# Optimization experiments

Hardware: AMD Instinct MI355X
Metric: run time of the kernel (lower is better)

## Reference

```python
import jax, jax.numpy as jnp
import numpy as np
import math

B, S, H, NH = 8, 2048, 256, 4
DH = H // NH
EPS = 1e-12


def setup_inputs() -> dict:
    key = jax.random.key(0)
    ks = jax.random.split(key, 20)
    g = lambda k, shape: (jax.random.normal(k, shape, jnp.float32) * 0.02)
    inp = {
        "hidden": jax.random.normal(ks[0], (B, S, H), jnp.float32),
        "Wq": g(ks[1], (H, H)), "bq": jnp.zeros((H,), jnp.float32),
        "Wk": g(ks[2], (H, H)), "bk": jnp.zeros((H,), jnp.float32),
        "Wv": g(ks[3], (H, H)), "bv": jnp.zeros((H,), jnp.float32),
        "Wo": g(ks[4], (H, H)), "bo": jnp.zeros((H,), jnp.float32),
        "W1": g(ks[5], (4 * H, H)), "b1": jnp.zeros((4 * H,), jnp.float32),
        "W2": g(ks[6], (H, 4 * H)), "b2": jnp.zeros((H,), jnp.float32),
        "ln1_w": jnp.ones((H,), jnp.float32), "ln1_b": jnp.zeros((H,), jnp.float32),
        "ln2_w": jnp.ones((H,), jnp.float32), "ln2_b": jnp.zeros((H,), jnp.float32),
        "mask": jax.random.randint(ks[7], (B, S), 0, 2, jnp.int32),
    }
    return inp


def _layernorm(x, w, b):
    u = x.mean(-1, keepdims=True)
    s = ((x - u) ** 2).mean(-1, keepdims=True)
    return w * (x - u) / jnp.sqrt(s + EPS) + b


def _gelu_tanh(h):
    return 0.5 * h * (1.0 + jnp.tanh(math.sqrt(2.0 / math.pi) * (h + 0.044715 * h ** 3)))


def _block(hidden, mask, Wq, bq, Wk, bk, Wv, bv, Wo, bo, W1, b1, W2, b2,
           ln1_w, ln1_b, ln2_w, ln2_b):
    # --- attention sublayer (pre-norm + residual) ---
    x = _layernorm(hidden, ln1_w, ln1_b)
    def heads(W, b):  # [B,S,H] -> [B,NH,S,DH]
        return (x @ W.T + b).reshape(B, S, NH, DH).transpose(0, 2, 1, 3)
    q, k, v = heads(Wq, bq), heads(Wk, bk), heads(Wv, bv)
    corr = jnp.einsum("bhqd,bhkd->bhqk", q, k) / math.sqrt(DH)
    # torch code masks QUERY rows: mask [B,S] broadcast over heads and keys
    corr = jnp.where(mask[:, None, :, None] == 0, -1e9, corr)
    prob = jax.nn.softmax(corr, axis=-1)
    attn = jnp.einsum("bhqk,bhkd->bhqd", prob, v)
    attn = attn.transpose(0, 2, 1, 3).reshape(B, S, H) @ Wo.T + bo
    hidden = hidden + attn
    # --- FFN sublayer (pre-norm + residual) ---
    y = _layernorm(hidden, ln2_w, ln2_b)
    h1 = y @ W1.T + b1
    ff = _gelu_tanh(h1) @ W2.T + b2
    return hidden + ff


def reference(hidden, Wq, bq, Wk, bk, Wv, bv, Wo, bo, W1, b1, W2, b2,
              ln1_w, ln1_b, ln2_w, ln2_b, mask):
    return _block(hidden, mask, Wq, bq, Wk, bk, Wv, bv, Wo, bo,
                  W1, b1, W2, b2, ln1_w, ln1_b, ln2_w, ln2_b)
```

## Files before the change

kernel.cpp:

```cpp
#include <hip/hip_runtime.h>
#include <hip/hip_bf16.h>
#include <cstdint>
#include <cstddef>

constexpr int CB  = 8;
constexpr int CS  = 2048;
constexpr int CH  = 256;
constexpr int CNH = 4;
constexpr int CDH = 64;
constexpr int CT  = CB * CS;

typedef __attribute__((ext_vector_type(8))) __bf16 bf16x8;
typedef __attribute__((ext_vector_type(4))) float  f32x4;

__device__ __forceinline__ float b2f(unsigned short u) {
    union { float f; unsigned int i; } v; v.i = ((unsigned int)u) << 16; return v.f;
}
__device__ __forceinline__ unsigned short f2b(float f) {
    union { float f; unsigned int i; } v; v.f = f;
    unsigned int r = v.i + 0x7FFFu + ((v.i >> 16) & 1u);
    return (unsigned short)(r >> 16);
}
__device__ __forceinline__ unsigned short f2b_fast(float f) {
    union { float f; unsigned int i; } v; v.f = f;
    return (unsigned short)((v.i + 0x8000u) >> 16);
}
__device__ __forceinline__ float fexp2(float x) {
#if __has_builtin(__builtin_amdgcn_exp2f)
    return __builtin_amdgcn_exp2f(x);
#else
    float r; asm("v_exp_f32 %0, %1" : "=v"(r) : "v"(x)); return r;
#endif
}
__device__ __forceinline__ f32x4 mfma16(bf16x8 a, bf16x8 b, f32x4 c) {
    return __builtin_amdgcn_mfma_f32_16x16x32_bf16(a, b, c, 0, 0, 0);
}

#define GLOAD_LDS16(gptr, lptr)                                                        \
    __builtin_amdgcn_global_load_lds((const __attribute__((address_space(1))) void*)(gptr), \
                                     (__attribute__((address_space(3))) void*)(lptr), 16, 0, 0)

#define QSCALE 0.1803368801111204f

__global__ __launch_bounds__(256) void detect_kernel(
    const unsigned short* __restrict__ h, int* __restrict__ flag)
{
    __shared__ int s_bad;
    const int tid = threadIdx.x;
    if (tid == 0) s_bad = 0;
    __syncthreads();
    bool bad = false;
    for (int i = tid; i < 2048; i += 256) {
        float v = b2f(h[i]);
        if (!(fabsf(v) < 1e25f)) bad = true;
    }
    if (bad) s_bad = 1;
    __syncthreads();
    if (tid == 0) *flag = s_bad;
}

struct CvtArgs6  { const void* src[6];  void* dst[6];  int n[6]; };
struct CvtArgs11 { const void* src[11]; void* dst[11]; int n[11]; };

__global__ __launch_bounds__(256) void cvt_to_bf16_k(const int* __restrict__ flag, CvtArgs6 a)
{
    const int seg = blockIdx.y, n = a.n[seg];
    const bool inf32 = (*flag != 0);
    const float* sf = (const float*)a.src[seg];
    const unsigned short* sb = (const unsigned short*)a.src[seg];
    unsigned short* d = (unsigned short*)a.dst[seg];
    for (int i = (blockIdx.x * 256 + threadIdx.x) * 4; i < n; i += gridDim.x * 1024) {
        ushort4 o;
        if (inf32) {
            float4 v = *(const float4*)(sf + i);
            o.x = f2b(v.x); o.y = f2b(v.y); o.z = f2b(v.z); o.w = f2b(v.w);
        } else {
            o = *(const ushort4*)(sb + i);
        }
        *(ushort4*)(d + i) = o;
    }
}

__global__ __launch_bounds__(256) void cvt_to_f32_k(const int* __restrict__ flag, CvtArgs11 a)
{
    const int seg = blockIdx.y, n = a.n[seg];
    const bool inf32 = (*flag != 0);
    const float* sf = (const float*)a.src[seg];
    const unsigned short* sb = (const unsigned short*)a.src[seg];
    float* d = (float*)a.dst[seg];
    for (int i = (blockIdx.x * 256 + threadIdx.x) * 4; i < n; i += gridDim.x * 1024) {
        float4 o;
        if (inf32) {
            o = *(const float4*)(sf + i);
        } else {
            ushort4 v = *(const ushort4*)(sb + i);
            o.x = b2f(v.x); o.y = b2f(v.y); o.z = b2f(v.z); o.w = b2f(v.w);
        }
        *(float4*)(d + i) = o;
    }
}

__global__ __launch_bounds__(256) void ln_kernel(
    const float* __restrict__ x, const float* __restrict__ w,
    const float* __restrict__ b, unsigned short* __restrict__ out)
{
    const int wave = threadIdx.x >> 6, lane = threadIdx.x & 63;
    const int token = blockIdx.x * 4 + wave;
    const int c = lane * 4;
    const size_t rowo = (size_t)token * CH + c;
    float4 u = *(const float4*)(x + rowo);
    float v0 = u.x, v1 = u.y, v2 = u.z, v3 = u.w;
    float s = v0 + v1 + v2 + v3;
    float q = v0*v0 + v1*v1 + v2*v2 + v3*v3;
    #pragma unroll
    for (int m = 1; m < 64; m <<= 1) { s += __shfl_xor(s, m, 64); q += __shfl_xor(q, m, 64); }
    float mean = s * (1.0f/256.0f);
    float var  = q * (1.0f/256.0f) - mean*mean;
    float inv  = rsqrtf(var + 1e-12f);
    float4 ww = *(const float4*)(w + c);
    float4 bb = *(const float4*)(b + c);
    ushort4 o;
    o.x = f2b(ww.x * (v0-mean)*inv + bb.x);
    o.y = f2b(ww.y * (v1-mean)*inv + bb.y);
    o.z = f2b(ww.z * (v2-mean)*inv + bb.z);
    o.w = f2b(ww.w * (v3-mean)*inv + bb.w);
    *(ushort4*)(out + rowo) = o;
}

template<bool GELU, bool RESID, bool HEADSTORE, bool OUTF32, bool OUTDYN>
__device__ __forceinline__ void gemm_core(
    const unsigned short* __restrict__ A, const unsigned short* __restrict__ W,
    const float* __restrict__ bias, const float* __restrict__ resid,
    void* __restrict__ out, const int* __restrict__ flag,
    int K, int N, int m0, int n0, float oscale)
{
    __shared__ __align__(16) unsigned short lA[128*32];
    __shared__ __align__(16) unsigned short lB[128*32];
    const int tid  = threadIdx.x;
    const int lane = tid & 63;
    const int wave = tid >> 6;
    const int wr = (wave >> 1) * 64;
    const int wc = (wave & 1) * 64;
    const int g = lane >> 4, r16 = lane & 15;
    const int lrow = lane >> 2;
    const int lch  = lane & 3;

    const f32x4 zero = {0.f, 0.f, 0.f, 0.f};
    f32x4 acc[4][4];
    #pragma unroll
    for (int m = 0; m < 4; ++m)
        #pragma unroll
        for (int n = 0; n < 4; ++n) acc[m][n] = zero;

    for (int k0 = 0; k0 < K; k0 += 32) {
        #pragma unroll
        for (int i = 0; i < 2; ++i) {
            int chunk = wave + i * 4;
            int row = chunk * 16 + lrow;
            const unsigned short* ga = A + (size_t)(m0 + row) * K + k0 + lch * 8;
            GLOAD_LDS16(ga, &lA[chunk * 512]);
            const unsigned short* gw = W + (size_t)(n0 + row) * K + k0 + lch * 8;
            GLOAD_LDS16(gw, &lB[chunk * 512]);
        }
        __syncthreads();
        bf16x8 af[4], wf[4];
        #pragma unroll
        for (int m = 0; m < 4; ++m) af[m] = *(const bf16x8*)&lA[(wr + m*16 + r16) * 32 + g * 8];
        #pragma unroll
        for (int n = 0; n < 4; ++n) wf[n] = *(const bf16x8*)&lB[(wc + n*16 + r16) * 32 + g * 8];
        #pragma unroll
        for (int m = 0; m < 4; ++m)
            #pragma unroll
            for (int n = 0; n < 4; ++n)
                acc[m][n] = mfma16(af[m], wf[n], acc[m][n]);
        __syncthreads();
    }

    const bool of32dyn = OUTDYN ? (*flag != 0) : false;
    #pragma unroll
    for (int n = 0; n < 4; ++n) {
        int col = n0 + wc + n*16 + r16;
        float bv = bias[col];
        #pragma unroll
        for (int m = 0; m < 4; ++m) {
            int row0 = m0 + wr + m*16 + g*4;
            #pragma unroll
            for (int r = 0; r < 4; ++r) {
                int row = row0 + r;
                float v = (acc[m][n][r] + bv) * oscale;
                if (GELU) {
                    float a = 0.79788456080286541f * (v + 0.044715f * v * v * v);
                    v = v * (1.0f / (1.0f + __expf(-2.0f * a)));
                }
                if (RESID) v += resid[(size_t)row * N + col];
                size_t oidx;
                if (HEADSTORE) {
                    int hh = col >> 6, d = col & 63;
                    int bb = row >> 11, ss = row & 2047;
                    oidx = ((((size_t)bb * CNH + hh) * CS) + ss) * CDH + d;
                } else {
                    oidx = (size_t)row * N + col;
                }
                if (OUTF32)      ((float*)out)[oidx] = v;
                else if (OUTDYN) {
                    if (of32dyn) ((float*)out)[oidx] = v;
                    else         ((unsigned short*)out)[oidx] = f2b(v);
                }
                else             ((unsigned short*)out)[oidx] = f2b(v);
            }
        }
    }
}

__global__ __launch_bounds__(256) void k_qkv(
    const unsigned short* __restrict__ xhat,
    const unsigned short* Wq, const float* bq, unsigned short* q,
    const unsigned short* Wk, const float* bk, unsigned short* k,
    const unsigned short* Wv, const float* bv, unsigned short* v)
{
    const unsigned short* W  = blockIdx.z == 0 ? Wq : (blockIdx.z == 1 ? Wk : Wv);
    const float*          bi = blockIdx.z == 0 ? bq : (blockIdx.z == 1 ? bk : bv);
    unsigned short*       o  = blockIdx.z == 0 ? q  : (blockIdx.z == 1 ? k  : v);
    const float osc = blockIdx.z == 0 ? QSCALE : 1.0f;
    gemm_core<false, false, true, false, false>(xhat, W, bi, nullptr, o, nullptr,
                                                CH, CH, blockIdx.x * 128, blockIdx.y * 128, osc);
}

__global__ __launch_bounds__(256) void k_oproj(
    const unsigned short* __restrict__ A, const unsigned short* __restrict__ W,
    const float* __restrict__ bias, const float* __restrict__ resid,
    float* __restrict__ out)
{
    gemm_core<false, true, false, true, false>(A, W, bias, resid, out, nullptr,
                                               CH, CH, blockIdx.x * 128, blockIdx.y * 128, 1.0f);
}

__global__ __launch_bounds__(256) void k_ffn1(
    const unsigned short* __restrict__ A, const unsigned short* __restrict__ W,
    const float* __restrict__ bias, unsigned short* __restrict__ out)
{
    gemm_core<true, false, false, false, false>(A, W, bias, nullptr, out, nullptr,
                                                CH, 4*CH, blockIdx.x * 128, blockIdx.y * 128, 1.0f);
}

__global__ __launch_bounds__(256) void k_ffn2(
    const unsigned short* __restrict__ A, const unsigned short* __restrict__ W,
    const float* __restrict__ bias, const float* __restrict__ resid,
    void* __restrict__ out, const int* __restrict__ flag)
{
    gemm_core<false, true, false, false, true>(A, W, bias, resid, out, flag,
                                               4*CH, CH, blockIdx.x * 128, blockIdx.y * 128, 1.0f);
}

__global__ __launch_bounds__(256) void vtrans_kernel(
    const unsigned short* __restrict__ v, unsigned short* __restrict__ vt)
{
    __shared__ unsigned short T[64 * 72];
    const int bh = blockIdx.y, s0 = blockIdx.x * 64, tid = threadIdx.x;
    const size_t ibase = (size_t)bh * CS * CDH;
    const size_t obase = (size_t)bh * CDH * CS;
    #pragma unroll
    for (int i = 0; i < 2; ++i) {
        int t2 = tid + i * 256;
        int row = t2 >> 3, ch = t2 & 7;
        uint4 dv = *(const uint4*)(v + ibase + (size_t)(s0 + row) * CDH + ch * 8);
        *(uint4*)&T[row * 72 + ch * 8] = dv;
    }
    __syncthreads();
    #pragma unroll
    for (int i = 0; i < 2; ++i) {
        int t2 = tid + i * 256;
        int d = t2 >> 3, ch = t2 & 7;
        unsigned short tmp[8];
        #pragma unroll
        for (int j = 0; j < 8; ++j) tmp[j] = T[(ch * 8 + j) * 72 + d];
        *(uint4*)(vt + obase + (size_t)d * CS + s0 + ch * 8) = *(uint4*)tmp;
    }
}

__global__ __launch_bounds__(512, 4) void attn_kernel(
    const unsigned short* __restrict__ Q, const unsigned short* __restrict__ Kp,
    const unsigned short* __restrict__ Vt, const int* __restrict__ mask,
    unsigned short* __restrict__ out)
{
    __shared__ __align__(16) unsigned short Qs[128 * 64];
    __shared__ __align__(16) unsigned short Ks[128 * 64];
    __shared__ __align__(16) unsigned short Vs[64 * 128];
    __shared__ __align__(16) unsigned short Ps[128 * 128];

    const int tid = threadIdx.x, lane = tid & 63, wave = tid >> 6;
    const int bh = blockIdx.y, bb = bh >> 2, hh = bh & 3;
    const int q0 = blockIdx.x * 128;
    const size_t baseQ = (size_t)bh * CS * CDH;
    const size_t baseT = (size_t)bh * CDH * CS;

    const int g = lane >> 4, r16 = lane & 15;
    const int wq = wave * 16;
    const int swz = (r16 & 7) << 4;

    #pragma unroll
    for (int i = 0; i < 2; ++i) {
        int t2 = tid + i * 512;
        int row = t2 >> 3, ch = t2 & 7;
        uint4 dv = *(const uint4*)(Q + baseQ + (size_t)(q0 + row) * CDH + ch * 8);
        if (mask[bb * CS + q0 + row] == 0) { dv.x = 0; dv.y = 0; dv.z = 0; dv.w = 0; }
        *(uint4*)((char*)Qs + row * 128 + ((ch * 16) ^ ((row & 7) << 4))) = dv;
    }

    f32x4 o_acc[4];
    float psum[4];
    #pragma unroll
    for (int n = 0; n < 4; ++n) o_acc[n] = (f32x4){0.f, 0.f, 0.f, 0.f};
    #pragma unroll
    for (int r = 0; r < 4; ++r) psum[r] = 0.f;

    const int kr0 = tid >> 3,  kc0 = tid & 7;
    const int kr1 = kr0 + 64;
    const int vd0 = tid >> 4,  vc0 = tid & 15;
    const int vd1 = vd0 + 32;
    char* kdstA = (char*)Ks + kr0 * 128 + ((kc0 * 16) ^ ((kr0 & 7) << 4));
    char* kdstB = (char*)Ks + kr1 * 128 + ((kc0 * 16) ^ ((kr1 & 7) << 4));
    char* vdstA = (char*)Vs + vd0 * 256 + ((vc0 * 16) ^ ((vd0 & 7) << 4));
    char* vdstB = (char*)Vs + vd1 * 256 + ((vc0 * 16) ^ ((vd1 & 7) << 4));

    uint4 kva, kvb, vva, vvb;
    kva = *(const uint4*)(Kp + baseQ + (size_t)kr0 * CDH + kc0 * 8);
    kvb = *(const uint4*)(Kp + baseQ + (size_t)kr1 * CDH + kc0 * 8);
    vva = *(const uint4*)(Vt + baseT + (size_t)vd0 * CS + vc0 * 8);
    vvb = *(const uint4*)(Vt + baseT + (size_t)vd1 * CS + vc0 * 8);

    for (int kt = 0; kt < CS; kt += 128) {
        *(uint4*)kdstA = kva;  *(uint4*)kdstB = kvb;
        *(uint4*)vdstA = vva;  *(uint4*)vdstB = vvb;
        __syncthreads();
        if (kt + 128 < CS) {
            kva = *(const uint4*)(Kp + baseQ + (size_t)(kt + 128 + kr0) * CDH + kc0 * 8);
            kvb = *(const uint4*)(Kp + baseQ + (size_t)(kt + 128 + kr1) * CDH + kc0 * 8);
            vva = *(const uint4*)(Vt + baseT + (size_t)vd0 * CS + (kt + 128) + vc0 * 8);
            vvb = *(const uint4*)(Vt + baseT + (size_t)vd1 * CS + (kt + 128) + vc0 * 8);
        }

        f32x4 s_acc[8];
        #pragma unroll
        for (int n = 0; n < 8; ++n) s_acc[n] = (f32x4){0.f, 0.f, 0.f, 0.f};
        __builtin_amdgcn_s_setprio(1);
        #pragma unroll
        for (int kk = 0; kk < 2; ++kk) {
            bf16x8 aq = *(const bf16x8*)((char*)Qs + (wq + r16) * 128 + ((kk*64 + g*16) ^ swz));
            #pragma unroll
            for (int n = 0; n < 8; ++n) {
                bf16x8 bk2 = *(const bf16x8*)((char*)Ks + (n*16 + r16) * 128 + ((kk*64 + g*16) ^ swz));
                s_acc[n] = mfma16(aq, bk2, s_acc[n]);
            }
        }
        __builtin_amdgcn_s_setprio(0);

        #pragma unroll
        for (int r = 0; r < 4; ++r) {
            const int rloc = wq + g * 4 + r;
            char* prow = (char*)Ps + rloc * 256;
            const int pswz = (rloc & 7) << 4;
            float acc = 0.f;
            #pragma unroll
            for (int n = 0; n < 8; ++n) {
                float p = fexp2(s_acc[n][r]);
                acc += p;
                *(unsigned short*)(prow + (((n*16 + r16) * 2) ^ pswz)) = f2b_fast(p);
            }
            psum[r] += acc;
        }

        __builtin_amdgcn_s_setprio(1);
        #pragma unroll
        for (int kk = 0; kk < 4; ++kk) {
            bf16x8 ap = *(const bf16x8*)((char*)Ps + (wq + r16) * 256 + ((kk*64 + g*16) ^ swz));
            #pragma unroll
            for (int n = 0; n < 4; ++n) {
                bf16x8 bv2 = *(const bf16x8*)((char*)Vs + (n*16 + r16) * 256 + ((kk*64 + g*16) ^ swz));
                o_acc[n] = mfma16(ap, bv2, o_acc[n]);
            }
        }
        __builtin_amdgcn_s_setprio(0);
        __syncthreads();
    }

    #pragma unroll
    for (int r = 0; r < 4; ++r) {
        float l = psum[r];
        #pragma unroll
        for (int d = 1; d < 16; d <<= 1) l += __shfl_xor(l, d, 64);
        float inv = 1.0f / l;
        const int rloc = wq + g * 4 + r;
        #pragma unroll
        for (int n = 0; n < 4; ++n)
            out[((size_t)(bb * CS + q0 + rloc)) * CH + hh * CDH + n*16 + r16] =
                f2b(o_acc[n][r] * inv);
    }
}

extern "C" void kernel_launch(void* const* d_in, const int* in_sizes, int n_in,
                              void* d_out, int out_size, void* d_ws, size_t ws_size,
                              hipStream_t stream)
{
    const void* hidden = d_in[0];
    const void* Wq = d_in[1];  const void* bq = d_in[2];
    const void* Wk = d_in[3];  const void* bk = d_in[4];
    const void* Wv = d_in[5];  const void* bv = d_in[6];
    const void* Wo = d_in[7];  const void* bo = d_in[8];
    const void* W1 = d_in[9];  const void* b1 = d_in[10];
    const void* W2 = d_in[11]; const void* b2 = d_in[12];
    const void* ln1w = d_in[13]; const void* ln1b = d_in[14];
    const void* ln2w = d_in[15]; const void* ln2b = d_in[16];
    const int* mask = (const int*)d_in[17];

    char* ws = (char*)d_ws;
    const size_t KB = 1u << 10, MB = 1u << 20;
    int*            flag  = (int*)ws;
    float*          bqf   = (float*)(ws + 4*KB);
    float*          bkf   = (float*)(ws + 8*KB);
    float*          bvf   = (float*)(ws + 12*KB);
    float*          bof   = (float*)(ws + 16*KB);
    float*          b1f   = (float*)(ws + 20*KB);
    float*          b2f_  = (float*)(ws + 28*KB);
    float*          ln1wf = (float*)(ws + 32*KB);
    float*          ln1bf = (float*)(ws + 36*KB);
    float*          ln2wf = (float*)(ws + 40*KB);
    float*          ln2bf = (float*)(ws + 44*KB);
    unsigned short* Wqb   = (unsigned short*)(ws + 1*MB);
    unsigned short* Wkb   = (unsigned short*)(ws + 1*MB + 256*KB);
    unsigned short* Wvb   = (unsigned short*)(ws + 1*MB + 512*KB);
    unsigned short* Wob   = (unsigned short*)(ws + 1*MB + 768*KB);
    unsigned short* W1b   = (unsigned short*)(ws + 2*MB);
    unsigned short* W2b   = (unsigned short*)(ws + 2*MB + 512*KB);
    float*          hf32  = (float*)(ws + 3*MB);
    unsigned short* xhat  = (unsigned short*)(ws + 19*MB);
    unsigned short* qb    = (unsigned short*)(ws + 27*MB);
    unsigned short* kb    = (unsigned short*)(ws + 35*MB);
    unsigned short* vb    = (unsigned short*)(ws + 43*MB);
    unsigned short* attnb = xhat;
    float*          hid2f = (float*)(ws + 35*MB);
    unsigned short* vtb   = (unsigned short*)(ws + 51*MB);
    unsigned short* yhat  = qb;
    unsigned short* h1g   = (unsigned short*)(ws + 51*MB);

    dim3 blk(256);
    detect_kernel<<<1, blk, 0, stream>>>((const unsigned short*)hidden, flag);

    CvtArgs6 cw;
    cw.src[0]=Wq;  cw.dst[0]=Wqb; cw.n[0]=CH*CH;
    cw.src[1]=Wk;  cw.dst[1]=Wkb; cw.n[1]=CH*CH;
    cw.src[2]=Wv;  cw.dst[2]=Wvb; cw.n[2]=CH*CH;
    cw.src[3]=Wo;  cw.dst[3]=Wob; cw.n[3]=CH*CH;
    cw.src[4]=W1;  cw.dst[4]=W1b; cw.n[4]=4*CH*CH;
    cw.src[5]=W2;  cw.dst[5]=W2b; cw.n[5]=4*CH*CH;
    cvt_to_bf16_k<<<dim3(64, 6), blk, 0, stream>>>(flag, cw);

    CvtArgs11 cf;
    cf.src[0]=hidden; cf.dst[0]=hf32;  cf.n[0]=CT*CH;
    cf.src[1]=bq;     cf.dst[1]=bqf;   cf.n[1]=CH;
    cf.src[2]=bk;     cf.dst[2]=bkf;   cf.n[2]=CH;
    cf.src[3]=bv;     cf.dst[3]=bvf;   cf.n[3]=CH;
    cf.src[4]=bo;     cf.dst[4]=bof;   cf.n[4]=CH;
    cf.src[5]=b1;     cf.dst[5]=b1f;   cf.n[5]=4*CH;
    cf.src[6]=b2;     cf.dst[6]=b2f_;  cf.n[6]=CH;
    cf.src[7]=ln1w;   cf.dst[7]=ln1wf; cf.n[7]=CH;
    cf.src[8]=ln1b;   cf.dst[8]=ln1bf; cf.n[8]=CH;
    cf.src[9]=ln2w;   cf.dst[9]=ln2wf; cf.n[9]=CH;
    cf.src[10]=ln2b;  cf.dst[10]=ln2bf;cf.n[10]=CH;
    cvt_to_f32_k<<<dim3(512, 11), blk, 0, stream>>>(flag, cf);

    ln_kernel<<<CT / 4, blk, 0, stream>>>(hf32, ln1wf, ln1bf, xhat);
    k_qkv<<<dim3(CT / 128, CH / 128, 3), blk, 0, stream>>>(xhat, Wqb, bqf, qb,
                                                           Wkb, bkf, kb, Wvb, bvf, vb);
    vtrans_kernel<<<dim3(CS / 64, CB * CNH), blk, 0, stream>>>(vb, vtb);
    attn_kernel<<<dim3(CS / 128, CB * CNH), dim3(512), 0, stream>>>(qb, kb, vtb, mask, attnb);
    k_oproj<<<dim3(CT / 128, CH / 128), blk, 0, stream>>>(attnb, Wob, bof, hf32, hid2f);
    ln_kernel<<<CT / 4, blk, 0, stream>>>(hid2f, ln2wf, ln2bf, yhat);
    k_ffn1<<<dim3(CT / 128, (4 * CH) / 128), blk, 0, stream>>>(yhat, W1b, b1f, h1g);
    k_ffn2<<<dim3(CT / 128, CH / 128), blk, 0, stream>>>(h1g, W2b, b2f_, hid2f,
                                                         d_out, flag);
}
```

Before: 173.2 us.

## Rewrite attention kernel with 32x32 MFMA, register P, and async LDS double buffering

Restructures the attention kernel to use 32x32x16 MFMAs, computing S^T so each wave keeps Q in registers. Waves are split into pairs sharing query rows, each pair covering half the key tile. P is repacked in registers with permlane32_swap instead of going through an LDS round trip. K and V tiles are double-buffered via global_load_lds direct-to-LDS copies. Partial O and row sums from the two key halves are combined through LDS at the end, which adds an epilogue reduction and changes the LDS layout to an unswizzled packed form that may cause bank conflicts.

```diff
diff --git a/kernel.cpp b/kernel.cpp
--- a/kernel.cpp
+++ b/kernel.cpp
@@ -10,8 +10,10 @@
 constexpr int CDH = 64;
 constexpr int CT  = CB * CS;
 
-typedef __attribute__((ext_vector_type(8))) __bf16 bf16x8;
-typedef __attribute__((ext_vector_type(4))) float  f32x4;
+typedef __attribute__((ext_vector_type(8)))  __bf16 bf16x8;
+typedef __attribute__((ext_vector_type(4)))  float  f32x4;
+typedef __attribute__((ext_vector_type(16))) float  f32x16;
+typedef __attribute__((ext_vector_type(2)))  int    i32x2;
 
 __device__ __forceinline__ float b2f(unsigned short u) {
     union { float f; unsigned int i; } v; v.i = ((unsigned int)u) << 16; return v.f;
@@ -24,6 +26,9 @@
 __device__ __forceinline__ unsigned short f2b_fast(float f) {
     union { float f; unsigned int i; } v; v.f = f;
     return (unsigned short)((v.i + 0x8000u) >> 16);
+}
+__device__ __forceinline__ unsigned int packbf(float a, float b) {
+    return (unsigned int)f2b_fast(a) | ((unsigned int)f2b_fast(b) << 16);
 }
 __device__ __forceinline__ float fexp2(float x) {
 #if __has_builtin(__builtin_amdgcn_exp2f)
@@ -34,6 +39,15 @@
 }
 __device__ __forceinline__ f32x4 mfma16(bf16x8 a, bf16x8 b, f32x4 c) {
     return __builtin_amdgcn_mfma_f32_16x16x32_bf16(a, b, c, 0, 0, 0);
+}
+__device__ __forceinline__ f32x16 mfma32(bf16x8 a, bf16x8 b, f32x16 c) {
+    return __builtin_amdgcn_mfma_f32_32x32x16_bf16(a, b, c, 0, 0, 0);
+}
+__device__ __forceinline__ f32x16 zero16() {
+    f32x16 z;
+    #pragma unroll
+    for (int i = 0; i < 16; ++i) z[i] = 0.f;
+    return z;
 }
 
 #define GLOAD_LDS16(gptr, lptr)                                                        \
@@ -283,119 +297,127 @@
     const unsigned short* __restrict__ Vt, const int* __restrict__ mask,
     unsigned short* __restrict__ out)
 {
-    __shared__ __align__(16) unsigned short Qs[128 * 64];
-    __shared__ __align__(16) unsigned short Ks[128 * 64];
-    __shared__ __align__(16) unsigned short Vs[64 * 128];
-    __shared__ __align__(16) unsigned short Ps[128 * 128];
+    __shared__ __align__(16) char lds[65536];
 
     const int tid = threadIdx.x, lane = tid & 63, wave = tid >> 6;
+    const int qb = wave >> 1, kh = wave & 1;
+    const int r32 = lane & 31, hi = lane >> 5;
     const int bh = blockIdx.y, bb = bh >> 2, hh = bh & 3;
     const int q0 = blockIdx.x * 128;
     const size_t baseQ = (size_t)bh * CS * CDH;
     const size_t baseT = (size_t)bh * CDH * CS;
 
-    const int g = lane >> 4, r16 = lane & 15;
-    const int wq = wave * 16;
-    const int swz = (r16 & 7) << 4;
-
-    #pragma unroll
-    for (int i = 0; i < 2; ++i) {
-        int t2 = tid + i * 512;
-        int row = t2 >> 3, ch = t2 & 7;
-        uint4 dv = *(const uint4*)(Q + baseQ + (size_t)(q0 + row) * CDH + ch * 8);
-        if (mask[bb * CS + q0 + row] == 0) { dv.x = 0; dv.y = 0; dv.z = 0; dv.w = 0; }
-        *(uint4*)((char*)Qs + row * 128 + ((ch * 16) ^ ((row & 7) << 4))) = dv;
-    }
-
-    f32x4 o_acc[4];
-    float psum[4];
-    #pragma unroll
-    for (int n = 0; n < 4; ++n) o_acc[n] = (f32x4){0.f, 0.f, 0.f, 0.f};
-    #pragma unroll
-    for (int r = 0; r < 4; ++r) psum[r] = 0.f;
-
-    const int kr0 = tid >> 3,  kc0 = tid & 7;
-    const int kr1 = kr0 + 64;
-    const int vd0 = tid >> 4,  vc0 = tid & 15;
-    const int vd1 = vd0 + 32;
-    char* kdstA = (char*)Ks + kr0 * 128 + ((kc0 * 16) ^ ((kr0 & 7) << 4));
-    char* kdstB = (char*)Ks + kr1 * 128 + ((kc0 * 16) ^ ((kr1 & 7) << 4));
-    char* vdstA = (char*)Vs + vd0 * 256 + ((vc0 * 16) ^ ((vd0 & 7) << 4));
-    char* vdstB = (char*)Vs + vd1 * 256 + ((vc0 * 16) ^ ((vd1 & 7) << 4));
-
-    uint4 kva, kvb, vva, vvb;
-    kva = *(const uint4*)(Kp + baseQ + (size_t)kr0 * CDH + kc0 * 8);
-    kvb = *(const uint4*)(Kp + baseQ + (size_t)kr1 * CDH + kc0 * 8);
-    vva = *(const uint4*)(Vt + baseT + (size_t)vd0 * CS + vc0 * 8);
-    vvb = *(const uint4*)(Vt + baseT + (size_t)vd1 * CS + vc0 * 8);
-
-    for (int kt = 0; kt < CS; kt += 128) {
-        *(uint4*)kdstA = kva;  *(uint4*)kdstB = kvb;
-        *(uint4*)vdstA = vva;  *(uint4*)vdstB = vvb;
+    const int qrow = q0 + qb * 32 + r32;
+    bf16x8 qf[4];
+    {
+        const bool live = (mask[bb * CS + qrow] != 0);
+        #pragma unroll
+        for (int dw = 0; dw < 4; ++dw) {
+            uint4 v = {0u, 0u, 0u, 0u};
+            if (live) v = *(const uint4*)(Q + baseQ + (size_t)qrow * CDH + dw * 16 + hi * 8);
+            qf[dw] = *(bf16x8*)&v;
+        }
+    }
+
+#define STAGE(BUF, KT) do {                                                             \
+        _Pragma("unroll")                                                               \
+        for (int i = 0; i < 2; ++i) {                                                   \
+            const int slot0 = i * 512 + wave * 64;                                      \
+            const int slot  = slot0 + lane;                                             \
+            const int kw = slot >> 7, kk2 = slot & 127;                                 \
+            GLOAD_LDS16(Kp + baseQ + (size_t)((KT) + kk2) * CDH + kw * 8,               \
+                        lds + (BUF) * 16384 + slot0 * 16);                              \
+            const int vc = slot >> 6, vd = slot & 63;                                   \
+            GLOAD_LDS16(Vt + baseT + (size_t)vd * CS + (KT) + vc * 8,                   \
+                        lds + 32768 + (BUF) * 16384 + slot0 * 16);                      \
+        } } while (0)
+
+    f32x16 o0 = zero16(), o1 = zero16();
+    float psum = 0.f;
+
+    STAGE(0, 0);
+    __syncthreads();
+
+    for (int t = 0; t < CS / 128; ++t) {
+        const int buf = t & 1;
+        const int kt = t * 128;
+        if (t + 1 < CS / 128) STAGE(buf ^ 1, kt + 128);
+
+        const char* kbase = lds + buf * 16384;
+        const char* vbase = lds + 32768 + buf * 16384;
+
+        f32x16 sT0 = zero16(), sT1 = zero16();
+        __builtin_amdgcn_s_setprio(1);
+        #pragma unroll
+        for (int dw = 0; dw < 4; ++dw) {
+            const char* cb = kbase + (dw * 2 + hi) * 2048;
+            bf16x8 k0 = *(const bf16x8*)(cb + (kh * 64 + r32) * 16);
+            bf16x8 k1 = *(const bf16x8*)(cb + (kh * 64 + 32 + r32) * 16);
+            sT0 = mfma32(k0, qf[dw], sT0);
+            sT1 = mfma32(k1, qf[dw], sT1);
+        }
+        __builtin_amdgcn_s_setprio(0);
+
+#define PROCKB(SREG, KB) do {                                                           \
+            float p[16];                                                                \
+            _Pragma("unroll")                                                           \
+            for (int r = 0; r < 16; ++r) { p[r] = fexp2((SREG)[r]); psum += p[r]; }     \
+            _Pragma("unroll")                                                           \
+            for (int w = 0; w < 2; ++w) {                                               \
+                unsigned int a01 = packbf(p[w*8+0], p[w*8+1]);                          \
+                unsigned int a23 = packbf(p[w*8+2], p[w*8+3]);                          \
+                unsigned int b01 = packbf(p[w*8+4], p[w*8+5]);                          \
+                unsigned int b23 = packbf(p[w*8+6], p[w*8+7]);                          \
+                unsigned int ap0, ap1, ap2, ap3;                                        \
+                {                                                                       \
+                    i32x2 s1 = __builtin_amdgcn_permlane32_swap((int)a01, (int)b01, false, false); \
+                    i32x2 s2 = __builtin_amdgcn_permlane32_swap((int)a23, (int)b23, false, false); \
+                    ap0 = (unsigned int)s1.x; ap2 = (unsigned int)s1.y;                 \
+                    ap1 = (unsigned int)s2.x; ap3 = (unsigned int)s2.y;                 \
+                }                                                                       \
+                union { unsigned int u[4]; bf16x8 v; } apv;                             \
+                apv.u[0] = ap0; apv.u[1] = ap1; apv.u[2] = ap2; apv.u[3] = ap3;         \
+                const char* vb2 = vbase + ((kh * 4 + (KB) * 2 + w) * 2 + hi) * 1024;    \
+                bf16x8 v0 = *(const bf16x8*)(vb2 + r32 * 16);                           \
+                bf16x8 v1 = *(const bf16x8*)(vb2 + (32 + r32) * 16);                    \
+                o0 = mfma32(apv.v, v0, o0);                                             \
+                o1 = mfma32(apv.v, v1, o1);                                             \
+            } } while (0)
+
+        PROCKB(sT0, 0);
+        PROCKB(sT1, 1);
+#undef PROCKB
+
         __syncthreads();
-        if (kt + 128 < CS) {
-            kva = *(const uint4*)(Kp + baseQ + (size_t)(kt + 128 + kr0) * CDH + kc0 * 8);
-            kvb = *(const uint4*)(Kp + baseQ + (size_t)(kt + 128 + kr1) * CDH + kc0 * 8);
-            vva = *(const uint4*)(Vt + baseT + (size_t)vd0 * CS + (kt + 128) + vc0 * 8);
-            vvb = *(const uint4*)(Vt + baseT + (size_t)vd1 * CS + (kt + 128) + vc0 * 8);
-        }
-
-        f32x4 s_acc[8];
-        #pragma unroll
-        for (int n = 0; n < 8; ++n) s_acc[n] = (f32x4){0.f, 0.f, 0.f, 0.f};
-        __builtin_amdgcn_s_setprio(1);
-        #pragma unroll
-        for (int kk = 0; kk < 2; ++kk) {
-            bf16x8 aq = *(const bf16x8*)((char*)Qs + (wq + r16) * 128 + ((kk*64 + g*16) ^ swz));
-            #pragma unroll
-            for (int n = 0; n < 8; ++n) {
-                bf16x8 bk2 = *(const bf16x8*)((char*)Ks + (n*16 + r16) * 128 + ((kk*64 + g*16) ^ swz));
-                s_acc[n] = mfma16(aq, bk2, s_acc[n]);
-            }
-        }
-        __builtin_amdgcn_s_setprio(0);
-
-        #pragma unroll
-        for (int r = 0; r < 4; ++r) {
-            const int rloc = wq + g * 4 + r;
-            char* prow = (char*)Ps + rloc * 256;
-            const int pswz = (rloc & 7) << 4;
-            float acc = 0.f;
-            #pragma unroll
-            for (int n = 0; n < 8; ++n) {
-                float p = fexp2(s_acc[n][r]);
-                acc += p;
-                *(unsigned short*)(prow + (((n*16 + r16) * 2) ^ pswz)) = f2b_fast(p);
-            }
-            psum[r] += acc;
-        }
-
-        __builtin_amdgcn_s_setprio(1);
-        #pragma unroll
-        for (int kk = 0; kk < 4; ++kk) {
-            bf16x8 ap = *(const bf16x8*)((char*)Ps + (wq + r16) * 256 + ((kk*64 + g*16) ^ swz));
-            #pragma unroll
-            for (int n = 0; n < 4; ++n) {
-                bf16x8 bv2 = *(const bf16x8*)((char*)Vs + (n*16 + r16) * 256 + ((kk*64 + g*16) ^ swz));
-                o_acc[n] = mfma16(ap, bv2, o_acc[n]);
-            }
-        }
-        __builtin_amdgcn_s_setprio(0);
-        __syncthreads();
-    }
-
-    #pragma unroll
-    for (int r = 0; r < 4; ++r) {
-        float l = psum[r];
-        #pragma unroll
-        for (int d = 1; d < 16; d <<= 1) l += __shfl_xor(l, d, 64);
-        float inv = 1.0f / l;
-        const int rloc = wq + g * 4 + r;
-        #pragma unroll
-        for (int n = 0; n < 4; ++n)
-            out[((size_t)(bb * CS + q0 + rloc)) * CH + hh * CDH + n*16 + r16] =
-                f2b(o_acc[n][r] * inv);
-    }
+    }
+
+    float ps = psum + __shfl_xor(psum, 32, 64);
+    float* lsum = (float*)(lds + 32768);
+    float* Oex  = (float*)lds;
+    if (lane < 32) lsum[(qb * 2 + kh) * 32 + r32] = ps;
+    if (kh == 1) {
+        #pragma unroll
+        for (int r = 0; r < 16; ++r) {
+            const int qr = (r & 3) + 8 * (r >> 2) + 4 * hi;
+            Oex[(qb * 32 + qr) * 64 + r32]      = o0[r];
+            Oex[(qb * 32 + qr) * 64 + 32 + r32] = o1[r];
+        }
+    }
+    __syncthreads();
+    if (kh == 0) {
+        #pragma unroll
+        for (int r = 0; r < 16; ++r) {
+            const int qr = (r & 3) + 8 * (r >> 2) + 4 * hi;
+            const float l = lsum[(qb * 2 + 0) * 32 + qr] + lsum[(qb * 2 + 1) * 32 + qr];
+            const float inv = 1.0f / l;
+            const float u0 = (o0[r] + Oex[(qb * 32 + qr) * 64 + r32]) * inv;
+            const float u1 = (o1[r] + Oex[(qb * 32 + qr) * 64 + 32 + r32]) * inv;
+            const size_t ob = (size_t)(bb * CS + q0 + qb * 32 + qr) * CH + hh * CDH;
+            out[ob + r32]      = f2b(u0);
+            out[ob + 32 + r32] = f2b(u1);
+        }
+    }
+#undef STAGE
 }
 
 extern "C" void kernel_launch(void* const* d_in, const int* in_sizes, int n_in,
```

New measurement: 167.8 us. -3.1%, faster.
